# Performance work log

Measured on AMD Instinct MI355X. Metric: run time of the kernel, lower is better.

## Reference

```python
import jax, jax.numpy as jnp
import numpy as np

N_NODES = 50000
N_HEDGES = 5000
NNZ = 800000
IN_C = 128
D1 = 256
D2 = D1 // 4  # 64


def setup_inputs() -> dict:
    key = jax.random.key(0)
    ks = jax.random.split(key, 7)
    x = jax.random.normal(ks[0], (N_NODES, IN_C), dtype=jnp.float32)
    node_idx = jax.random.randint(ks[1], (NNZ,), 0, N_NODES, dtype=jnp.int32)
    hedge_idx = jax.random.randint(ks[2], (NNZ,), 0, N_HEDGES, dtype=jnp.int32)
    edge = jnp.stack([node_idx, hedge_idx], axis=0)  # [2, nnz]
    W1 = jax.random.normal(ks[3], (IN_C, D1), dtype=jnp.float32) / np.float32(np.sqrt(IN_C))
    b1 = jnp.zeros((D1,), dtype=jnp.float32)
    W2 = jax.random.normal(ks[4], (D1, D2), dtype=jnp.float32) / np.float32(np.sqrt(D1))
    b2 = jnp.zeros((D2,), dtype=jnp.float32)
    return {"x": x, "edge": edge, "W1": W1, "b1": b1, "W2": W2, "b2": b2}


def _hconv(x, W, b, node_idx, hedge_idx):
    # HypergraphConv (no attention, unit hyperedge weights):
    # out = D^{-1} H B^{-1} H^T (X W) + b
    xw = x @ W  # [N, F]
    ones = jnp.ones((node_idx.shape[0],), dtype=xw.dtype)
    deg = jax.ops.segment_sum(ones, node_idx, num_segments=N_NODES)      # D_i
    Dinv = jnp.where(deg > 0, 1.0 / deg, 0.0)
    cnt = jax.ops.segment_sum(ones, hedge_idx, num_segments=N_HEDGES)    # B_e
    Binv = jnp.where(cnt > 0, 1.0 / cnt, 0.0)
    # node -> hyperedge aggregation (gather + segment_sum), normalized by B^{-1}
    e = jax.ops.segment_sum(xw[node_idx], hedge_idx, num_segments=N_HEDGES) * Binv[:, None]
    # hyperedge -> node aggregation, normalized by D^{-1}
    out = jax.ops.segment_sum(e[hedge_idx], node_idx, num_segments=N_NODES) * Dinv[:, None]
    return out + b


def reference(x, edge, W1, b1, W2, b2):
    node_idx, hedge_idx = edge[0], edge[1]
    h = jax.nn.relu(_hconv(x, W1, b1, node_idx, hedge_idx))
    out = jax.nn.relu(_hconv(h, W2, b2, node_idx, hedge_idx))
    return out
```

## Files before the change

### kernel.cpp

```cpp
#include <hip/hip_runtime.h>

#define N_NODES 50000
#define N_HEDGES 5000
#define NNZ 800000
#define IN_C 128
#define D1 256
#define D2 64
#define SN 64
#define SH 256

#define HBK 20
#define NHB 250
#define HCAP 4096
#define NBK 100
#define NNB 500
#define NCAP 2048
#define BKT_BLOCKS ((NNZ + 2047) / 2048)

typedef unsigned int u32;
typedef unsigned short u16;
typedef __attribute__((ext_vector_type(8))) short short8;
typedef __attribute__((ext_vector_type(4))) float f32x4;

__device__ __forceinline__ float bf_lo(u32 u) { return __uint_as_float(u << 16); }
__device__ __forceinline__ float bf_hi(u32 u) { return __uint_as_float(u & 0xffff0000u); }
__device__ __forceinline__ u32 rne16(float f) {
    u32 u = __float_as_uint(f);
    return (u + 0x7fffu + ((u >> 16) & 1u)) >> 16;
}
__device__ __forceinline__ u32 pack2(float a, float b) {
    return rne16(a) | (rne16(b) << 16);
}
__device__ __forceinline__ void acc8(float* a, uint4 v) {
    a[0] += bf_lo(v.x); a[1] += bf_hi(v.x);
    a[2] += bf_lo(v.y); a[3] += bf_hi(v.y);
    a[4] += bf_lo(v.z); a[5] += bf_hi(v.z);
    a[6] += bf_lo(v.w); a[7] += bf_hi(v.w);
}

__global__ void cast_bucket(const float4* __restrict__ x, uint2* __restrict__ xb,
                            const float* __restrict__ W1, u16* __restrict__ w1hi,
                            u16* __restrict__ w1lo,
                            const float* __restrict__ W2, u16* __restrict__ w2hi,
                            u16* __restrict__ w2lo,
                            const int* __restrict__ nidx, const int* __restrict__ hidx,
                            int* __restrict__ gcur_h, int* __restrict__ gcur_n,
                            u32* __restrict__ pairs_h, u32* __restrict__ pairs_n) {
    __shared__ int hist_h[NHB], hist_n[NNB];
    __shared__ int base_h[NHB], base_n[NNB];
    int tid = threadIdx.x;
    int i = blockIdx.x * 256 + tid;
    float4 v = x[i];
    uint2 o;
    o.x = pack2(v.x, v.y);
    o.y = pack2(v.z, v.w);
    xb[i] = o;
    if (i < 32768) {
        int j = i & 7;
        int l = (i >> 3) & 63;
        int ct = (i >> 9) & 15;
        int kc = i >> 13;
        int k = kc * 32 + (l >> 4) * 8 + j;
        int n = ct * 16 + (l & 15);
        float w = W1[k * D1 + n];
        u32 h = rne16(w);
        w1hi[i] = (u16)h;
        w1lo[i] = (u16)rne16(w - bf_lo(h));
    } else if (i < 32768 + 16384) {
        int t = i - 32768;
        int j = t & 7;
        int l = (t >> 3) & 63;
        int nt = (t >> 9) & 3;
        int kc = t >> 11;
        int k = kc * 32 + (l >> 4) * 8 + j;
        int n = nt * 16 + (l & 15);
        float w = W2[k * D2 + n];
        u32 h = rne16(w);
        w2hi[t] = (u16)h;
        w2lo[t] = (u16)rne16(w - bf_lo(h));
    }
    if (blockIdx.x >= BKT_BLOCKS) return;
    for (int t = tid; t < NHB; t += 256) hist_h[t] = 0;
    for (int t = tid; t < NNB; t += 256) hist_n[t] = 0;
    __syncthreads();
    int e0 = blockIdx.x * 2048 + tid * 8;
    int ns[8], hs_[8];
#pragma unroll
    for (int k = 0; k < 8; k++) {
        int e = e0 + k;
        if (e < NNZ) {
            ns[k] = nidx[e];
            hs_[k] = hidx[e];
            atomicAdd(&hist_h[hs_[k] / HBK], 1);
            atomicAdd(&hist_n[ns[k] / NBK], 1);
        } else {
            ns[k] = -1;
        }
    }
    __syncthreads();
    if (tid < NHB) base_h[tid] = atomicAdd(&gcur_h[tid], hist_h[tid]);
    for (int t = tid; t < NNB; t += 256) base_n[t] = atomicAdd(&gcur_n[t], hist_n[t]);
    __syncthreads();
    for (int t = tid; t < NHB; t += 256) hist_h[t] = 0;
    for (int t = tid; t < NNB; t += 256) hist_n[t] = 0;
    __syncthreads();
#pragma unroll
    for (int k = 0; k < 8; k++) {
        if (ns[k] >= 0) {
            int n = ns[k], h = hs_[k];
            int bh = h / HBK, bn = n / NBK;
            int s1 = base_h[bh] + atomicAdd(&hist_h[bh], 1);
            if (s1 < HCAP) pairs_h[bh * HCAP + s1] = ((u32)h << 16) | (u32)n;
            int s2 = base_n[bn] + atomicAdd(&hist_n[bn], 1);
            if (s2 < NCAP) pairs_n[bn * NCAP + s2] = ((u32)n << 16) | (u32)h;
        }
    }
}

__global__ void build_adj(const u32* __restrict__ pairs_h, const int* __restrict__ gcur_h,
                          u16* __restrict__ adj_h, int* __restrict__ cur_h,
                          const u32* __restrict__ pairs_n, const int* __restrict__ gcur_n,
                          u16* __restrict__ adj_n, int* __restrict__ cur_n) {
    __shared__ u16 rows[NBK * SN];
    __shared__ int cnt[NBK];
    int tid = threadIdx.x;
    if (blockIdx.x < NHB) {
        int b = blockIdx.x;
        if (tid < HBK) cnt[tid] = 0;
        __syncthreads();
        int np = gcur_h[b];
        if (np > HCAP) np = HCAP;
        for (int t = tid; t < np; t += 256) {
            u32 p = pairs_h[b * HCAP + t];
            int hl = (int)(p >> 16) - b * HBK;
            int s = atomicAdd(&cnt[hl], 1);
            if (s < SH) rows[hl * SH + s] = (u16)(p & 0xffff);
        }
        __syncthreads();
        u32* dst = (u32*)(adj_h + b * HBK * SH);
        const u32* srcl = (const u32*)rows;
        for (int t = tid; t < HBK * SH / 2; t += 256) dst[t] = srcl[t];
        if (tid < HBK) cur_h[b * HBK + tid] = cnt[tid];
    } else {
        int b = blockIdx.x - NHB;
        if (tid < NBK) cnt[tid] = 0;
        __syncthreads();
        int np = gcur_n[b];
        if (np > NCAP) np = NCAP;
        for (int t = tid; t < np; t += 256) {
            u32 p = pairs_n[b * NCAP + t];
            int nl = (int)(p >> 16) - b * NBK;
            int s = atomicAdd(&cnt[nl], 1);
            if (s < SN) rows[nl * SN + s] = (u16)(p & 0xffff);
        }
        __syncthreads();
        u32* dst = (u32*)(adj_n + b * NBK * SN);
        const u32* srcl = (const u32*)rows;
        for (int t = tid; t < NBK * SN / 2; t += 256) dst[t] = srcl[t];
        if (tid < NBK) cur_n[b * NBK + tid] = cnt[tid];
    }
}

template <int F, int S, int SPLIT>
__global__ void gather_split(const uint4* __restrict__ src, const int* __restrict__ cur,
                             const u16* __restrict__ adj, uint4* __restrict__ dst,
                             int nrows) {
    constexpr int L = F / 8;
    constexpr int TR = L * SPLIT;
    constexpr int RB = 256 / TR;
    constexpr int CHUNK = S / SPLIT;
    int tid = threadIdx.x;
    int rl = tid / TR;
    int seg = (tid % TR) / L;
    int c = tid % L;
    int row = blockIdx.x * RB + rl;
    bool valid = row < nrows;
    int len = valid ? cur[row] : 0;
    int lenc = (len < S) ? len : S;
    int js = seg * CHUNK;
    int je = (lenc < js + CHUNK) ? lenc : (js + CHUNK);
    float a0[8] = {0,0,0,0,0,0,0,0}, a1[8] = {0,0,0,0,0,0,0,0};
    float a2[8] = {0,0,0,0,0,0,0,0}, a3[8] = {0,0,0,0,0,0,0,0};
    if (valid) {
        const u16* arow = adj + row * S;
        int j = js;
        for (; j + 7 < je; j += 8) {
            uint4 aa = *(const uint4*)(arow + j);
            int i0 = aa.x & 0xffff, i1 = aa.x >> 16;
            int i2 = aa.y & 0xffff, i3 = aa.y >> 16;
            int i4 = aa.z & 0xffff, i5 = aa.z >> 16;
            int i6 = aa.w & 0xffff, i7 = aa.w >> 16;
            uint4 v0 = src[i0 * L + c];
            uint4 v1 = src[i1 * L + c];
            uint4 v2 = src[i2 * L + c];
            uint4 v3 = src[i3 * L + c];
            uint4 v4 = src[i4 * L + c];
            uint4 v5 = src[i5 * L + c];
            uint4 v6 = src[i6 * L + c];
            uint4 v7 = src[i7 * L + c];
            acc8(a0, v0); acc8(a1, v1); acc8(a2, v2); acc8(a3, v3);
            acc8(a0, v4); acc8(a1, v5); acc8(a2, v6); acc8(a3, v7);
        }
        for (; j < je; j++) {
            uint4 v = src[(int)arow[j] * L + c];
            acc8(a0, v);
        }
    }
    __shared__ float partf[256][8];
#pragma unroll
    for (int t = 0; t < 8; t++) partf[tid][t] = ((a0[t] + a1[t]) + (a2[t] + a3[t]));
    __syncthreads();
    if (seg == 0 && valid) {
        float r[8];
#pragma unroll
        for (int t = 0; t < 8; t++) r[t] = partf[tid][t];
#pragma unroll
        for (int s2 = 1; s2 < SPLIT; s2++) {
#pragma unroll
            for (int t = 0; t < 8; t++) r[t] += partf[tid + s2 * L][t];
        }
        float inv = (len > 0) ? 1.f / (float)len : 0.f;
        uint4 o;
        o.x = pack2(r[0] * inv, r[1] * inv);
        o.y = pack2(r[2] * inv, r[3] * inv);
        o.z = pack2(r[4] * inv, r[5] * inv);
        o.w = pack2(r[6] * inv, r[7] * inv);
        dst[row * L + c] = o;
    }
}

template <int F, int S, bool BIAS_RELU, bool DST_BF16>
__global__ void gatherb(const uint4* __restrict__ src, const int* __restrict__ cur,
                        const u16* __restrict__ adj, const float4* __restrict__ bias,
                        void* __restrict__ dst, int nrows) {
    constexpr int L = F / 8;
    int gid = blockIdx.x * 256 + threadIdx.x;
    int row = gid / L;
    if (row >= nrows) return;
    int c = gid - row * L;
    int len = cur[row];
    int lenc = (len < S) ? len : S;
    int s = row * S, e = s + lenc;
    float a0[8] = {0,0,0,0,0,0,0,0}, a1[8] = {0,0,0,0,0,0,0,0};
    float a2[8] = {0,0,0,0,0,0,0,0}, a3[8] = {0,0,0,0,0,0,0,0};
    int j = s;
    for (; j + 7 < e; j += 8) {
        uint4 aa = *(const uint4*)(adj + j);
        int i0 = aa.x & 0xffff, i1 = aa.x >> 16;
        int i2 = aa.y & 0xffff, i3 = aa.y >> 16;
        int i4 = aa.z & 0xffff, i5 = aa.z >> 16;
        int i6 = aa.w & 0xffff, i7 = aa.w >> 16;
        uint4 v0 = src[i0 * L + c];
        uint4 v1 = src[i1 * L + c];
        uint4 v2 = src[i2 * L + c];
        uint4 v3 = src[i3 * L + c];
        uint4 v4 = src[i4 * L + c];
        uint4 v5 = src[i5 * L + c];
        uint4 v6 = src[i6 * L + c];
        uint4 v7 = src[i7 * L + c];
        acc8(a0, v0); acc8(a1, v1); acc8(a2, v2); acc8(a3, v3);
        acc8(a0, v4); acc8(a1, v5); acc8(a2, v6); acc8(a3, v7);
    }
    for (; j < e; j++) {
        uint4 v = src[(int)adj[j] * L + c];
        acc8(a0, v);
    }
    float inv = (len > 0) ? 1.f / (float)len : 0.f;
    float r[8];
#pragma unroll
    for (int t = 0; t < 8; t++) r[t] = ((a0[t] + a1[t]) + (a2[t] + a3[t])) * inv;
    if (BIAS_RELU) {
        float4 b0 = bias[c * 2], b1v = bias[c * 2 + 1];
        r[0] = fmaxf(r[0] + b0.x, 0.f); r[1] = fmaxf(r[1] + b0.y, 0.f);
        r[2] = fmaxf(r[2] + b0.z, 0.f); r[3] = fmaxf(r[3] + b0.w, 0.f);
        r[4] = fmaxf(r[4] + b1v.x, 0.f); r[5] = fmaxf(r[5] + b1v.y, 0.f);
        r[6] = fmaxf(r[6] + b1v.z, 0.f); r[7] = fmaxf(r[7] + b1v.w, 0.f);
    }
    if (DST_BF16) {
        uint4 o;
        o.x = pack2(r[0], r[1]);
        o.y = pack2(r[2], r[3]);
        o.z = pack2(r[4], r[5]);
        o.w = pack2(r[6], r[7]);
        ((uint4*)dst)[row * L + c] = o;
    } else {
        float4* d = (float4*)dst;
        d[row * (F / 4) + c * 2]     = make_float4(r[0], r[1], r[2], r[3]);
        d[row * (F / 4) + c * 2 + 1] = make_float4(r[4], r[5], r[6], r[7]);
    }
}

#define SB_STRIDE 136
#define HSTRIDE 264
__global__ __launch_bounds__(256, 3)
void gather_mlp(const uint4* __restrict__ aggxb4, const int* __restrict__ cur_n,
                const u16* __restrict__ adj_n,
                const short8* __restrict__ w1hi, const short8* __restrict__ w1lo,
                const float* __restrict__ b1,
                const short8* __restrict__ w2hi, const short8* __restrict__ w2lo,
                u16* __restrict__ hw) {
    __shared__ u16 sbs[64 * SB_STRIDE];
    __shared__ u16 hs[64 * HSTRIDE];
    int tid = threadIdx.x;
    int node0 = blockIdx.x * 64;
    {
        int c = tid & 15;
        int nlb = tid >> 4;
#pragma unroll
        for (int rep = 0; rep < 4; rep++) {
            int nl = nlb + rep * 16;
            int node = node0 + nl;
            int len = (node < N_NODES) ? cur_n[node] : 0;
            int lenc = (len < SN) ? len : SN;
            const u16* adj = adj_n + node * SN;
            float a0[8] = {0,0,0,0,0,0,0,0}, a1[8] = {0,0,0,0,0,0,0,0};
            float a2[8] = {0,0,0,0,0,0,0,0}, a3[8] = {0,0,0,0,0,0,0,0};
            int j = 0;
            for (; j + 7 < lenc; j += 8) {
                uint4 aa = *(const uint4*)(adj + j);
                int i0 = aa.x & 0xffff, i1 = aa.x >> 16;
                int i2 = aa.y & 0xffff, i3 = aa.y >> 16;
                int i4 = aa.z & 0xffff, i5 = aa.z >> 16;
                int i6 = aa.w & 0xffff, i7 = aa.w >> 16;
                uint4 v0 = aggxb4[i0 * 16 + c];
                uint4 v1 = aggxb4[i1 * 16 + c];
                uint4 v2 = aggxb4[i2 * 16 + c];
                uint4 v3 = aggxb4[i3 * 16 + c];
                uint4 v4 = aggxb4[i4 * 16 + c];
                uint4 v5 = aggxb4[i5 * 16 + c];
                uint4 v6 = aggxb4[i6 * 16 + c];
                uint4 v7 = aggxb4[i7 * 16 + c];
                acc8(a0, v0); acc8(a1, v1); acc8(a2, v2); acc8(a3, v3);
                acc8(a0, v4); acc8(a1, v5); acc8(a2, v6); acc8(a3, v7);
            }
            for (; j < lenc; j++) {
                uint4 v = aggxb4[(int)adj[j] * 16 + c];
                acc8(a0, v);
            }
            float inv = (len > 0) ? 1.f / (float)len : 0.f;
            float r[8];
#pragma unroll
            for (int t = 0; t < 8; t++) r[t] = ((a0[t] + a1[t]) + (a2[t] + a3[t])) * inv;
            u32* dstl = (u32*)&sbs[nl * SB_STRIDE + c * 8];
            dstl[0] = pack2(r[0], r[1]);
            dstl[1] = pack2(r[2], r[3]);
            dstl[2] = pack2(r[4], r[5]);
            dstl[3] = pack2(r[6], r[7]);
        }
    }
    __syncthreads();
    int wave = tid >> 6;
    int lane = tid & 63;
    int m = lane & 15;
    int q = lane >> 4;
    float bc[4];
#pragma unroll
    for (int i = 0; i < 4; i++) bc[i] = b1[(wave * 4 + i) * 16 + m];
    f32x4 acc[4][4];
#pragma unroll
    for (int i = 0; i < 4; i++)
#pragma unroll
        for (int mt = 0; mt < 4; mt++)
            acc[i][mt] = (f32x4){bc[i], bc[i], bc[i], bc[i]};
#pragma unroll
    for (int kc = 0; kc < 4; kc++) {
        short8 am[4];
#pragma unroll
        for (int mt = 0; mt < 4; mt++)
            am[mt] = *(const short8*)&sbs[(mt * 16 + m) * SB_STRIDE + kc * 32 + q * 8];
        short8 whi[4], wlo[4];
#pragma unroll
        for (int i = 0; i < 4; i++) {
            whi[i] = w1hi[(kc * 16 + wave * 4 + i) * 64 + lane];
            wlo[i] = w1lo[(kc * 16 + wave * 4 + i) * 64 + lane];
        }
#pragma unroll
        for (int i = 0; i < 4; i++)
#pragma unroll
            for (int mt = 0; mt < 4; mt++) {
                acc[i][mt] = __builtin_amdgcn_mfma_f32_16x16x32_bf16(am[mt], whi[i], acc[i][mt], 0, 0, 0);
                acc[i][mt] = __builtin_amdgcn_mfma_f32_16x16x32_bf16(am[mt], wlo[i], acc[i][mt], 0, 0, 0);
            }
    }
#pragma unroll
    for (int i = 0; i < 4; i++) {
        int col = (wave * 4 + i) * 16 + m;
#pragma unroll
        for (int mt = 0; mt < 4; mt++)
#pragma unroll
            for (int r = 0; r < 4; r++) {
                float h = fmaxf(acc[i][mt][r], 0.f);
                hs[(mt * 16 + q * 4 + r) * HSTRIDE + col] = (u16)rne16(h);
            }
    }
    __syncthreads();
    f32x4 acc2[4];
#pragma unroll
    for (int mt = 0; mt < 4; mt++) acc2[mt] = (f32x4){0.f, 0.f, 0.f, 0.f};
#pragma unroll
    for (int kc = 0; kc < 8; kc++) {
        short8 ah[4];
#pragma unroll
        for (int mt = 0; mt < 4; mt++)
            ah[mt] = *(const short8*)&hs[(mt * 16 + m) * HSTRIDE + kc * 32 + q * 8];
        short8 whi = w2hi[(kc * 4 + wave) * 64 + lane];
        short8 wlo = w2lo[(kc * 4 + wave) * 64 + lane];
#pragma unroll
        for (int mt = 0; mt < 4; mt++) {
            acc2[mt] = __builtin_amdgcn_mfma_f32_16x16x32_bf16(ah[mt], whi, acc2[mt], 0, 0, 0);
            acc2[mt] = __builtin_amdgcn_mfma_f32_16x16x32_bf16(ah[mt], wlo, acc2[mt], 0, 0, 0);
        }
    }
#pragma unroll
    for (int mt = 0; mt < 4; mt++)
#pragma unroll
        for (int r = 0; r < 4; r++) {
            int row = node0 + mt * 16 + q * 4 + r;
            if (row < N_NODES)
                hw[row * D2 + wave * 16 + m] = (u16)rne16(acc2[mt][r]);
        }
}

extern "C" void kernel_launch(void* const* d_in, const int* in_sizes, int n_in,
                              void* d_out, int out_size, void* d_ws, size_t ws_size,
                              hipStream_t stream) {
    const float* x  = (const float*)d_in[0];
    const int* edge = (const int*)d_in[1];
    const int* nidx = edge;
    const int* hidx = edge + NNZ;
    const float* W1 = (const float*)d_in[2];
    const float* b1 = (const float*)d_in[3];
    const float* W2 = (const float*)d_in[4];
    const float* b2 = (const float*)d_in[5];
    float* out = (float*)d_out;

    u16* xb     = (u16*)d_ws;
    u16* aggxb  = xb + N_NODES * IN_C;
    u16* hwb    = aggxb + N_HEDGES * IN_C;
    u16* e2b    = hwb + N_NODES * D2;
    u16* w1hi   = e2b + N_HEDGES * D2;
    u16* w1lo   = w1hi + 32768;
    u16* w2hi   = w1lo + 32768;
    u16* w2lo   = w2hi + 16384;
    u16* adj_n  = w2lo + 16384;
    u16* adj_h  = adj_n + N_NODES * SN;
    u32* pairs_h = (u32*)(adj_h + N_HEDGES * SH);
    u32* pairs_n = pairs_h + NHB * HCAP;
    int* cur_n  = (int*)(pairs_n + NNB * NCAP);
    int* cur_h  = cur_n + N_NODES;
    int* gcur_h = cur_h + N_HEDGES;
    int* gcur_n = gcur_h + 256;

    hipMemsetAsync(gcur_h, 0, (256 + 512) * sizeof(int), stream);

    cast_bucket<<<N_NODES * IN_C / 4 / 256, 256, 0, stream>>>(
        (const float4*)x, (uint2*)xb, W1, w1hi, w1lo, W2, w2hi, w2lo,
        nidx, hidx, gcur_h, gcur_n, pairs_h, pairs_n);

    build_adj<<<NHB + NNB, 256, 0, stream>>>(pairs_h, gcur_h, adj_h, cur_h,
                                             pairs_n, gcur_n, adj_n, cur_n);

    gather_split<IN_C, SH, 4><<<(N_HEDGES + 3) / 4, 256, 0, stream>>>(
        (const uint4*)xb, cur_h, adj_h, (uint4*)aggxb, N_HEDGES);

    gather_mlp<<<(N_NODES + 63) / 64, 256, 0, stream>>>(
        (const uint4*)aggxb, cur_n, adj_n,
        (const short8*)w1hi, (const short8*)w1lo, b1,
        (const short8*)w2hi, (const short8*)w2lo, hwb);

    gather_split<D2, SH, 8><<<(N_HEDGES + 3) / 4, 256, 0, stream>>>(
        (const uint4*)hwb, cur_h, adj_h, (uint4*)e2b, N_HEDGES);
    gatherb<D2, SN, true, false><<<(N_NODES * (D2 / 8) + 255) / 256, 256, 0, stream>>>(
        (const uint4*)e2b, cur_n, adj_n, (const float4*)b2, out, N_NODES);
}
```

Before: 225.4 us.

## Split fused gather+MLP kernel into separate gather and MFMA MLP kernels

Unfuses the hyperedge-to-node gather from the MLP kernel: a generic gatherb kernel writes the aggregated bf16 rows to a global workspace, and a new mlp64 kernel reads them directly from global memory for the MFMA matmuls. This drops the shared staging buffer so the MLP kernel can raise occupancy (launch bounds 4), and lets the gather run with its own finer-grained thread mapping. In exchange it adds a global write and re-read of a 50000x128 bf16 intermediate plus an extra kernel launch. The MLP A-operand loads now come from global memory instead of LDS.

```diff
diff --git a/kernel.cpp b/kernel.cpp
--- a/kernel.cpp
+++ b/kernel.cpp
@@ -290,84 +290,34 @@
     }
 }
 
-#define SB_STRIDE 136
 #define HSTRIDE 264
-__global__ __launch_bounds__(256, 3)
-void gather_mlp(const uint4* __restrict__ aggxb4, const int* __restrict__ cur_n,
-                const u16* __restrict__ adj_n,
-                const short8* __restrict__ w1hi, const short8* __restrict__ w1lo,
-                const float* __restrict__ b1,
-                const short8* __restrict__ w2hi, const short8* __restrict__ w2lo,
-                u16* __restrict__ hw) {
-    __shared__ u16 sbs[64 * SB_STRIDE];
+__global__ __launch_bounds__(256, 4)
+void mlp64(const u16* __restrict__ sb,
+           const short8* __restrict__ w1hi, const short8* __restrict__ w1lo,
+           const float* __restrict__ b1,
+           const short8* __restrict__ w2hi, const short8* __restrict__ w2lo,
+           u16* __restrict__ hw) {
     __shared__ u16 hs[64 * HSTRIDE];
     int tid = threadIdx.x;
     int node0 = blockIdx.x * 64;
-    {
-        int c = tid & 15;
-        int nlb = tid >> 4;
-#pragma unroll
-        for (int rep = 0; rep < 4; rep++) {
-            int nl = nlb + rep * 16;
-            int node = node0 + nl;
-            int len = (node < N_NODES) ? cur_n[node] : 0;
-            int lenc = (len < SN) ? len : SN;
-            const u16* adj = adj_n + node * SN;
-            float a0[8] = {0,0,0,0,0,0,0,0}, a1[8] = {0,0,0,0,0,0,0,0};
-            float a2[8] = {0,0,0,0,0,0,0,0}, a3[8] = {0,0,0,0,0,0,0,0};
-            int j = 0;
-            for (; j + 7 < lenc; j += 8) {
-                uint4 aa = *(const uint4*)(adj + j);
-                int i0 = aa.x & 0xffff, i1 = aa.x >> 16;
-                int i2 = aa.y & 0xffff, i3 = aa.y >> 16;
-                int i4 = aa.z & 0xffff, i5 = aa.z >> 16;
-                int i6 = aa.w & 0xffff, i7 = aa.w >> 16;
-                uint4 v0 = aggxb4[i0 * 16 + c];
-                uint4 v1 = aggxb4[i1 * 16 + c];
-                uint4 v2 = aggxb4[i2 * 16 + c];
-                uint4 v3 = aggxb4[i3 * 16 + c];
-                uint4 v4 = aggxb4[i4 * 16 + c];
-                uint4 v5 = aggxb4[i5 * 16 + c];
-                uint4 v6 = aggxb4[i6 * 16 + c];
-                uint4 v7 = aggxb4[i7 * 16 + c];
-                acc8(a0, v0); acc8(a1, v1); acc8(a2, v2); acc8(a3, v3);
-                acc8(a0, v4); acc8(a1, v5); acc8(a2, v6); acc8(a3, v7);
-            }
-            for (; j < lenc; j++) {
-                uint4 v = aggxb4[(int)adj[j] * 16 + c];
-                acc8(a0, v);
-            }
-            float inv = (len > 0) ? 1.f / (float)len : 0.f;
-            float r[8];
-#pragma unroll
-            for (int t = 0; t < 8; t++) r[t] = ((a0[t] + a1[t]) + (a2[t] + a3[t])) * inv;
-            u32* dstl = (u32*)&sbs[nl * SB_STRIDE + c * 8];
-            dstl[0] = pack2(r[0], r[1]);
-            dstl[1] = pack2(r[2], r[3]);
-            dstl[2] = pack2(r[4], r[5]);
-            dstl[3] = pack2(r[6], r[7]);
-        }
-    }
-    __syncthreads();
     int wave = tid >> 6;
     int lane = tid & 63;
     int m = lane & 15;
     int q = lane >> 4;
-    float bc[4];
-#pragma unroll
-    for (int i = 0; i < 4; i++) bc[i] = b1[(wave * 4 + i) * 16 + m];
     f32x4 acc[4][4];
 #pragma unroll
-    for (int i = 0; i < 4; i++)
+    for (int i = 0; i < 4; i++) {
+        float bc = b1[(wave * 4 + i) * 16 + m];
 #pragma unroll
         for (int mt = 0; mt < 4; mt++)
-            acc[i][mt] = (f32x4){bc[i], bc[i], bc[i], bc[i]};
+            acc[i][mt] = (f32x4){bc, bc, bc, bc};
+    }
 #pragma unroll
     for (int kc = 0; kc < 4; kc++) {
         short8 am[4];
 #pragma unroll
         for (int mt = 0; mt < 4; mt++)
-            am[mt] = *(const short8*)&sbs[(mt * 16 + m) * SB_STRIDE + kc * 32 + q * 8];
+            am[mt] = *(const short8*)&sb[(node0 + mt * 16 + m) * IN_C + kc * 32 + q * 8];
         short8 whi[4], wlo[4];
 #pragma unroll
         for (int i = 0; i < 4; i++) {
@@ -450,6 +400,7 @@
     int* cur_h  = cur_n + N_NODES;
     int* gcur_h = cur_h + N_HEDGES;
     int* gcur_n = gcur_h + 256;
+    u16* sb     = (u16*)(gcur_n + 512);
 
     hipMemsetAsync(gcur_h, 0, (256 + 512) * sizeof(int), stream);
 
@@ -463,9 +414,11 @@
     gather_split<IN_C, SH, 4><<<(N_HEDGES + 3) / 4, 256, 0, stream>>>(
         (const uint4*)xb, cur_h, adj_h, (uint4*)aggxb, N_HEDGES);
 
-    gather_mlp<<<(N_NODES + 63) / 64, 256, 0, stream>>>(
-        (const uint4*)aggxb, cur_n, adj_n,
-        (const short8*)w1hi, (const short8*)w1lo, b1,
+    gatherb<IN_C, SN, false, true><<<(N_NODES * (IN_C / 8) + 255) / 256, 256, 0, stream>>>(
+        (const uint4*)aggxb, cur_n, adj_n, (const float4*)b1, (void*)sb, N_NODES);
+
+    mlp64<<<(N_NODES + 63) / 64, 256, 0, stream>>>(
+        sb, (const short8*)w1hi, (const short8*)w1lo, b1,
         (const short8*)w2hi, (const short8*)w2lo, hwb);
 
     gather_split<D2, SH, 8><<<(N_HEDGES + 3) / 4, 256, 0, stream>>>(
```

Result: no change. 225.4 us (-0.0%).
